# Kernel optimization log

Measured on AMD Instinct MI355X. Metric: run time of the kernel, lower is better.

Reference implementation:

```python
import jax, jax.numpy as jnp
import numpy as np

B, J, C = 256, 21, 256   # batch, joints, in_dim
H, D = 8, 256            # heads, out_dim (=hidden)
L, K = 2, 8              # layers, knn_k


def _knn_idx(coords, k):
    # coords: (B,J,3). Squared distances give same ordering as cdist p=2.
    d2 = jnp.sum((coords[:, :, None, :] - coords[:, None, :, :]) ** 2, axis=-1)  # (B,J,J)
    order = jnp.argsort(d2, axis=-1)
    return order[..., 1:k + 1]  # drop self -> (B,J,K)


def _mhgat(x, nbr_idx, wq, wk, wv, wp):
    b, j, _ = x.shape
    q = (x @ wq).reshape(b, j, H, D)
    k = (x @ wk).reshape(b, j, H, D)
    v = (x @ wv).reshape(b, j, H, D)
    bi = jnp.arange(b)[:, None, None]
    k_nbr = k[bi, nbr_idx]  # (B,J,K,H,D) gather of neighbor keys
    v_nbr = v[bi, nbr_idx]  # (B,J,K,H,D)
    attn = jnp.einsum('bjhd,bjkhd->bjkh', q, k_nbr) / np.float32(np.sqrt(D))
    attn = jax.nn.leaky_relu(attn, negative_slope=0.2)
    attn = jax.nn.softmax(attn, axis=2)  # over K neighbors
    out = jnp.einsum('bjkh,bjkhd->bjhd', attn, v_nbr).reshape(b, j, H * D)
    return out @ wp  # (B,J,hidden)


def setup_inputs() -> dict:
    key = jax.random.key(0)
    ks = jax.random.split(key, 9)
    s_in = 1.0 / np.sqrt(C)
    s_hd = 1.0 / np.sqrt(H * D)
    s_h = 1.0 / np.sqrt(D)
    joint_feats = jax.random.normal(ks[0], (B, J, C), jnp.float32)
    # layer-stacked weights (in_dim == hidden == 256 so both layers stack)
    wq = jax.random.normal(ks[1], (L, C, H * D), jnp.float32) * s_in
    wk = jax.random.normal(ks[2], (L, C, H * D), jnp.float32) * s_in
    wv = jax.random.normal(ks[3], (L, C, H * D), jnp.float32) * s_in
    wp = jax.random.normal(ks[4], (L, H * D, D), jnp.float32) * s_hd
    ws = jax.random.normal(ks[5], (L, C, D), jnp.float32) * s_in
    wskip0 = jax.random.normal(ks[6], (C, D), jnp.float32) * s_in
    fc_w = jax.random.normal(ks[7], (D, 3), jnp.float32) * s_h
    fc_b = jax.random.normal(ks[8], (3,), jnp.float32) * s_h
    return {"joint_feats": joint_feats, "wq": wq, "wk": wk, "wv": wv,
            "wp": wp, "ws": ws, "wskip0": wskip0, "fc_w": fc_w, "fc_b": fc_b}


def reference(joint_feats, wq, wk, wv, wp, ws, wskip0, fc_w, fc_b):
    h0 = joint_feats
    h = h0
    stats = []
    for l in range(L):
        nbr_idx = _knn_idx(jax.lax.stop_gradient(h[..., :3]), K)  # dynamic kNN graph
        out = _mhgat(h, nbr_idx, wq[l], wk[l], wv[l], wp[l])
        h = jax.nn.relu(out + h @ ws[l] + h0 @ wskip0)
        stats.append(jnp.abs(h).mean())
    coords = h @ fc_w + fc_b
    alphas = jnp.mean(jnp.stack(stats))
    return coords, alphas
```

## Files before the change

kernel.cpp:

```cpp
#include <hip/hip_runtime.h>
#include <hip/hip_bf16.h>
#include <math.h>
#include <type_traits>

namespace {
constexpr int Bb = 256, Jj = 21, Cc = 256, Hh = 8, Dd = 256;
constexpr int Mrows = Bb * Jj;
constexpr int HD    = Hh * Dd;
constexpr int QKVN  = 3 * HD;
constexpr int KNN   = 8;
constexpr int KFUSE = HD + Cc + Cc;

constexpr size_t OFF_QKV   = 0;
constexpr size_t OFF_T     = OFF_QKV   + (size_t)Mrows*QKVN*2;
constexpr size_t OFF_ATT   = OFF_T     + (size_t)Mrows*HD*4;
constexpr size_t OFF_GT    = OFF_ATT   + (size_t)Mrows*HD*2;
constexpr size_t OFF_G1T   = OFF_GT    + (size_t)HD*768*2;
constexpr size_t OFF_JFB   = OFF_G1T   + (size_t)HD*Cc*2;
constexpr size_t OFF_JFH   = OFF_JFB   + (size_t)Mrows*Cc*2;
constexpr size_t OFF_JFL   = OFF_JFH   + (size_t)Mrows*Cc*2;
constexpr size_t OFF_JFD   = OFF_JFL   + (size_t)Mrows*Cc*2;
constexpr size_t OFF_H1B   = OFF_JFD   + (size_t)Mrows*Cc*2;
constexpr size_t OFF_H2F   = OFF_H1B   + (size_t)Mrows*Cc*2;
constexpr size_t OFF_WQKVT = OFF_H2F   + (size_t)Mrows*Cc*4;
constexpr size_t OFF_FBT   = OFF_WQKVT + (size_t)2*QKVN*Cc*2;
constexpr size_t OFF_WVP   = OFF_FBT   + (size_t)2*Cc*KFUSE*2;
constexpr size_t OFF_VPROJ = OFF_WVP   + (size_t)Cc*24*4;
constexpr size_t OFF_WSUM  = OFF_VPROJ + (size_t)Mrows*24*4;
constexpr size_t OFF_CRD   = OFF_WSUM  + (size_t)Cc*4*4;
constexpr size_t OFF_NBR0  = OFF_CRD   + (size_t)Mrows*4*4;
constexpr size_t OFF_NBR1  = OFF_NBR0  + (size_t)Mrows*KNN*4;
constexpr size_t OFF_STAT  = OFF_NBR1  + (size_t)Mrows*KNN*4;
}

typedef short short8 __attribute__((ext_vector_type(8)));
typedef _Float16 half8 __attribute__((ext_vector_type(8)));
typedef _Float16 half4v __attribute__((ext_vector_type(4)));
typedef unsigned short u16x8 __attribute__((ext_vector_type(8)));
typedef float f32x4 __attribute__((ext_vector_type(4)));

__device__ __forceinline__ unsigned short f2bf(float x) {
    unsigned int u = __float_as_uint(x);
    u = u + 0x7fffu + ((u >> 16) & 1u);
    return (unsigned short)(u >> 16);
}
__device__ __forceinline__ float bf2f(unsigned short b) {
    return __uint_as_float(((unsigned int)b) << 16);
}

__device__ __forceinline__ void knn_body(int b, const float* __restrict__ src,
                                         int ld, int* __restrict__ nbr,
                                         float (*cs)[3]) {
    int t = threadIdx.x;
    if (t < Jj) {
        const float* p = src + (size_t)(b * Jj + t) * ld;
        cs[t][0] = p[0]; cs[t][1] = p[1]; cs[t][2] = p[2];
    }
    __syncthreads();
    if (t < Jj) {
        float x = cs[t][0], y = cs[t][1], z = cs[t][2];
        float d2[Jj];
        #pragma unroll
        for (int jj = 0; jj < Jj; ++jj) {
            float dx = x - cs[jj][0], dy = y - cs[jj][1], dz = z - cs[jj][2];
            d2[jj] = dx*dx + dy*dy + dz*dz;
        }
        unsigned int used = 0u;
        int out_base = (b * Jj + t) * KNN;
        #pragma unroll
        for (int r = 0; r <= KNN; ++r) {
            int best = -1; float bd = INFINITY;
            #pragma unroll
            for (int jj = 0; jj < Jj; ++jj)
                if (!((used >> jj) & 1u) && d2[jj] < bd) { bd = d2[jj]; best = jj; }
            used |= (1u << best);
            if (r > 0) nbr[out_base + r - 1] = best;
        }
    }
}

__device__ __forceinline__ void g_gemm_body(const float* __restrict__ wq,
                                            const float* __restrict__ wk,
                                            int h, int m0, int n0, char* sm,
                                            float acc[2][4]) {
    float (*As)[36] = (float(*)[36])sm;
    float (*Ws)[68] = (float(*)[68])(sm + 4608);
    int tidx = threadIdx.x;
    int ty = tidx >> 4, tx = tidx & 15;
    for (int kb = 0; kb < 256; kb += 32) {
        {
            int row = tidx >> 3, col = (tidx & 7) * 4;
            float4 v = *(const float4*)&wq[(size_t)(m0 + row)*HD + h*256 + kb + col];
            As[col+0][row] = v.x; As[col+1][row] = v.y;
            As[col+2][row] = v.z; As[col+3][row] = v.w;
            int row2 = tidx >> 2, col2 = (tidx & 3) * 8;
            float4 u0 = *(const float4*)&wk[(size_t)(n0 + row2)*HD + h*256 + kb + col2];
            float4 u1 = *(const float4*)&wk[(size_t)(n0 + row2)*HD + h*256 + kb + col2 + 4];
            Ws[col2+0][row2] = u0.x; Ws[col2+1][row2] = u0.y;
            Ws[col2+2][row2] = u0.z; Ws[col2+3][row2] = u0.w;
            Ws[col2+4][row2] = u1.x; Ws[col2+5][row2] = u1.y;
            Ws[col2+6][row2] = u1.z; Ws[col2+7][row2] = u1.w;
        }
        __syncthreads();
        #pragma unroll
        for (int kk = 0; kk < 32; ++kk) {
            float a0 = As[kk][ty*2], a1 = As[kk][ty*2 + 1];
            float4 bv = *(const float4*)&Ws[kk][tx*4];
            float b4[4] = {bv.x, bv.y, bv.z, bv.w};
            #pragma unroll
            for (int j = 0; j < 4; ++j) {
                acc[0][j] += a0 * b4[j];
                acc[1][j] += a1 * b4[j];
            }
        }
        __syncthreads();
    }
}

__global__ __launch_bounds__(256)
void mega_prep_kernel(const float* __restrict__ jf,
                      const float* __restrict__ wq, const float* __restrict__ wk,
                      const float* __restrict__ wv, const float* __restrict__ wp,
                      const float* __restrict__ wsw, const float* __restrict__ wsk,
                      unsigned short* __restrict__ wqkvT,
                      unsigned short* __restrict__ fbt, float* __restrict__ stats,
                      float* __restrict__ wsum,
                      unsigned short* __restrict__ jfb, _Float16* __restrict__ jfh,
                      _Float16* __restrict__ jfl, _Float16* __restrict__ jfd,
                      _Float16* __restrict__ GT, unsigned short* __restrict__ G1T,
                      float* __restrict__ Wvp2, int* __restrict__ nbr0) {
    __shared__ __align__(16) char sm[17408];
    int bid = blockIdx.x;
    int tidx = threadIdx.x;
    constexpr size_t CH = (size_t)Cc * HD;

    if (bid < 256) {
        int h = bid >> 5, rem = bid & 31;
        int m0 = (rem >> 2) * 32, n0 = (rem & 3) * 64;
        int ty = tidx >> 4, tx = tidx & 15;
        float acc[2][4] = {};
        g_gemm_body(wq, wk, h, m0, n0, sm, acc);
        #pragma unroll
        for (int j = 0; j < 4; ++j) {
            int n = h*256 + n0 + tx*4 + j;
            float g0 = acc[0][j], g1 = acc[1][j];
            _Float16 h0_ = (_Float16)g0, h1_ = (_Float16)g1;
            _Float16* base = &GT[(size_t)n*768 + m0 + ty*2];
            base[0]   = h0_;                          base[1]   = h1_;
            base[256] = (_Float16)(g0 * 0.0625f);     base[257] = (_Float16)(g1 * 0.0625f);
            base[512] = (_Float16)((g0 - (float)h0_) * 128.0f);
            base[513] = (_Float16)((g1 - (float)h1_) * 128.0f);
        }
    } else if (bid < 512) {
        int q = bid - 256;
        int h = q >> 5, rem = q & 31;
        int m0 = (rem >> 2) * 32, n0 = (rem & 3) * 64;
        int ty = tidx >> 4, tx = tidx & 15;
        float acc[2][4] = {};
        g_gemm_body(wq + CH, wk + CH, h, m0, n0, sm, acc);
        #pragma unroll
        for (int j = 0; j < 4; ++j) {
            int n = h*256 + n0 + tx*4 + j;
            unsigned short* base = &G1T[(size_t)n*256 + m0 + ty*2];
            base[0] = f2bf(acc[0][j]);
            base[1] = f2bf(acc[1][j]);
        }
    } else if (bid < 520) {
        int h = bid - 512;
        float (*wpc)[3] = (float(*)[3])sm;
        int t = tidx;
        const float* p = &wp[(size_t)(h*256 + t) * Cc];
        wpc[t][0] = p[0]; wpc[t][1] = p[1]; wpc[t][2] = p[2];
        __syncthreads();
        const float* vr = &wv[(size_t)t*HD + h*256];
        float a0=0, a1=0, a2=0;
        for (int d = 0; d < 256; ++d) {
            float v = vr[d];
            a0 += v*wpc[d][0]; a1 += v*wpc[d][1]; a2 += v*wpc[d][2];
        }
        float* o = &Wvp2[(size_t)t*24 + h*3];
        o[0]=a0; o[1]=a1; o[2]=a2;
    } else if (bid < 776) {
        knn_body(bid - 520, jf, Cc, nbr0, (float(*)[3])sm);
    } else if (bid == 776) {
        int e = tidx;
        float4 o;
        o.x = wsw[(size_t)e*Dd + 0] + wsk[(size_t)e*Dd + 0];
        o.y = wsw[(size_t)e*Dd + 1] + wsk[(size_t)e*Dd + 1];
        o.z = wsw[(size_t)e*Dd + 2] + wsk[(size_t)e*Dd + 2];
        o.w = 0.0f;
        *(float4*)&wsum[e*4] = o;
        if (e < 2) stats[e] = 0.0f;
    } else if (bid < 2121) {
        int i = (bid - 777) * 256 + tidx;
        float4 v = ((const float4*)jf)[i];
        float x[4] = {v.x, v.y, v.z, v.w};
        ushort4 ob; half4v oh, ol, od;
        #pragma unroll
        for (int u = 0; u < 4; ++u) {
            ((unsigned short*)&ob)[u] = f2bf(x[u]);
            _Float16 h = (_Float16)x[u];
            oh[u] = h;
            ol[u] = (_Float16)((x[u] - (float)h) * 16.0f);
            od[u] = (_Float16)(x[u] * 0.0078125f);
        }
        ((ushort4*)jfb)[i] = ob;
        ((half4v*)jfh)[i] = oh;
        ((half4v*)jfl)[i] = ol;
        ((half4v*)jfd)[i] = od;
    } else {
        int tt = bid - 2121;
        const float* src; unsigned short* dst;
        int ldin, ldout, tilesX, tile;
        if (tt < 2048) {
            int opIdx = tt >> 9; tile = tt & 511; tilesX = 64;
            int op = (opIdx < 3) ? opIdx : 5;
            ldin = HD; ldout = Cc;
            const float* s3[3] = {wq, wk, wv};
            src = s3[op % 3] + (size_t)(op / 3) * CH;
            dst = wqkvT + (size_t)(op % 3) * HD * Cc + (size_t)(op / 3) * QKVN * Cc;
        } else if (tt < 3072) {
            int op = (tt - 2048) >> 9; tile = (tt - 2048) & 511; tilesX = 8;
            ldin = Cc; ldout = KFUSE;
            src = wp + (size_t)op * HD * Cc;
            dst = fbt + (size_t)op * Cc * KFUSE;
        } else {
            int q = tt - 3072; int op = q >> 6; tile = q & 63; tilesX = 8;
            ldin = Cc; ldout = KFUSE;
            const float* s4[4] = {wsw, wsw + (size_t)Cc * Cc, wsk, wsk};
            src = s4[op];
            dst = fbt + (size_t)(op & 1) * Cc * KFUSE + HD + (size_t)(op >> 1) * Cc;
        }
        int bx = tile % tilesX, by = tile / tilesX;
        int n0 = bx * 32, k0 = by * 32;
        float (*t)[33] = (float(*)[33])sm;
        int r = tidx >> 3, c4 = (tidx & 7) * 4;
        float4 v = *(const float4*)&src[(size_t)(k0 + r) * ldin + n0 + c4];
        t[r][c4+0] = v.x; t[r][c4+1] = v.y; t[r][c4+2] = v.z; t[r][c4+3] = v.w;
        __syncthreads();
        ushort4 o;
        o.x = f2bf(t[c4+0][r]); o.y = f2bf(t[c4+1][r]);
        o.z = f2bf(t[c4+2][r]); o.w = f2bf(t[c4+3][r]);
        *(ushort4*)&dst[(size_t)(n0 + r) * ldout + k0 + c4] = o;
    }
}

template<int BM, int BN, int BK, int NSEG, bool RELU_STATS, bool OUT_BF16, bool F16>
__device__ __forceinline__
void gemm_core(unsigned short* As, unsigned short* Bs, float* red,
               int bm, int bn,
               const unsigned short* __restrict__ A0, int lda0, int klen0,
               const unsigned short* __restrict__ A1, int lda1, int klen1,
               const unsigned short* __restrict__ A2, int lda2, int klen2,
               const unsigned short* __restrict__ Bt, int ldb,
               void* __restrict__ Cv, int ldc, float* __restrict__ stat) {
    constexpr int WM = BM/2, WN = BN/2;
    constexpr int MW = WM/16, NW = WN/16, KW = BK/32;
    constexpr int CHUNKA = BM*BK/8;
    constexpr int CHUNKB = BN*BK/8;
    constexpr int KB8 = BK/8;
    constexpr int SWZ = KB8 - 1;
    using frag = std::conditional_t<F16, half8, short8>;

    int tid = threadIdx.x;
    int wid = tid >> 6, lane = tid & 63;
    int wr = wid >> 1, wc = wid & 1;

    f32x4 acc[MW][NW];
    #pragma unroll
    for (int m = 0; m < MW; ++m)
        #pragma unroll
        for (int n = 0; n < NW; ++n)
            acc[m][n] = (f32x4){0.f, 0.f, 0.f, 0.f};

    const unsigned short* Aseg[3] = {A0, A1, A2};
    const int ldas[3] = {lda0, lda1, lda2};
    const int klens[3] = {klen0, klen1, klen2};

    int kglob = 0;
    for (int seg = 0; seg < NSEG; ++seg) {
        const unsigned short* A = Aseg[seg];
        const int lda = ldas[seg];
        const int klen = klens[seg];
        for (int k0 = 0; k0 < klen; k0 += BK) {
            #pragma unroll
            for (int it = 0; it < CHUNKA/256; ++it) {
                int c = tid + it*256;
                int row = c / KB8;
                int kp = (c % KB8) ^ (row & SWZ);
                __builtin_amdgcn_global_load_lds(
                    (const __attribute__((address_space(1))) unsigned int*)
                        (A + (size_t)(bm + row)*lda + k0 + kp*8),
                    (__attribute__((address_space(3))) unsigned int*)(As + c*8),
                    16, 0, 0);
            }
            #pragma unroll
            for (int it = 0; it < CHUNKB/256; ++it) {
                int c = tid + it*256;
                int row = c / KB8;
                int kp = (c % KB8) ^ (row & SWZ);
                __builtin_amdgcn_global_load_lds(
                    (const __attribute__((address_space(1))) unsigned int*)
                        (Bt + (size_t)(bn + row)*ldb + kglob + k0 + kp*8),
                    (__attribute__((address_space(3))) unsigned int*)(Bs + c*8),
                    16, 0, 0);
            }
            __syncthreads();
            #pragma unroll
            for (int kp = 0; kp < KW; ++kp) {
                frag af[MW], bf[NW];
                int cbase = kp*4 + (lane >> 4);
                #pragma unroll
                for (int m = 0; m < MW; ++m) {
                    int r = wr*WM + m*16 + (lane & 15);
                    af[m] = *(const frag*)&As[r*BK + ((cbase ^ (r & SWZ))*8)];
                }
                #pragma unroll
                for (int n = 0; n < NW; ++n) {
                    int r = wc*WN + n*16 + (lane & 15);
                    bf[n] = *(const frag*)&Bs[r*BK + ((cbase ^ (r & SWZ))*8)];
                }
                #pragma unroll
                for (int m = 0; m < MW; ++m)
                    #pragma unroll
                    for (int n = 0; n < NW; ++n) {
                        if constexpr (F16)
                            acc[m][n] = __builtin_amdgcn_mfma_f32_16x16x32_f16(
                                af[m], bf[n], acc[m][n], 0, 0, 0);
                        else
                            acc[m][n] = __builtin_amdgcn_mfma_f32_16x16x32_bf16(
                                af[m], bf[n], acc[m][n], 0, 0, 0);
                    }
            }
            __syncthreads();
        }
        kglob += klen;
    }

    int cr = (lane >> 4)*4, cc = lane & 15;
    float bsum = 0.0f;
    #pragma unroll
    for (int m = 0; m < MW; ++m)
        #pragma unroll
        for (int n = 0; n < NW; ++n)
            #pragma unroll
            for (int j = 0; j < 4; ++j) {
                float v = acc[m][n][j];
                if (RELU_STATS) { v = fmaxf(v, 0.0f); bsum += v; }
                size_t row = bm + wr*WM + m*16 + cr + j;
                size_t col = bn + wc*WN + n*16 + cc;
                if (OUT_BF16) ((unsigned short*)Cv)[row*ldc + col] = f2bf(v);
                else          ((float*)Cv)[row*ldc + col] = v;
            }
    if (RELU_STATS) {
        #pragma unroll
        for (int sft = 1; sft < 64; sft <<= 1) bsum += __shfl_xor(bsum, sft);
        if (lane == 0) red[wid] = bsum;
        __syncthreads();
        if (tid == 0) atomicAdd(stat, red[0] + red[1] + red[2] + red[3]);
    }
}

__global__ __launch_bounds__(256)
void combo_kernel(const unsigned short* __restrict__ jfb,
                  const unsigned short* __restrict__ wqkvT,
                  unsigned short* __restrict__ QKVb,
                  const _Float16* __restrict__ jfh, const _Float16* __restrict__ jfl,
                  const _Float16* __restrict__ jfd, const _Float16* __restrict__ GT,
                  float* __restrict__ Tm,
                  const float* __restrict__ jf, const float* __restrict__ Wvp2,
                  float* __restrict__ vproj) {
    __shared__ __align__(16) char smem[32784];
    unsigned short* As = (unsigned short*)smem;
    unsigned short* Bs = (unsigned short*)(smem + 16384);
    float* red = (float*)(smem + 32768);
    int x = blockIdx.x, y = blockIdx.y;
    if (y < 16) {
        int lb = x + 42*y;
        int nb = (lb & 7) * 84 + (lb >> 3);
        int sx = nb % 42, sy = nb / 42;
        gemm_core<128,128,64,1,false,true,false>(As, Bs, red, sx*128,
            2*HD + sy*128,
            jfb, Cc, Cc, jfb, Cc, 0, jfb, Cc, 0, wqkvT, Cc, QKVb, QKVN, nullptr);
    } else if (y < 32) {
        int lb = x + 42*(y - 16);
        int nb = (lb & 7) * 84 + (lb >> 3);
        int sx = nb / 16, sy = nb % 16;
        gemm_core<128,128,64,3,false,false,true>(As, Bs, red, sx*128, sy*128,
            (const unsigned short*)jfh, Cc, Cc, (const unsigned short*)jfl, Cc, Cc,
            (const unsigned short*)jfd, Cc, Cc, (const unsigned short*)GT, 768,
            Tm, HD, nullptr);
    } else {
        int q = (y - 32) * 42 + x;
        float (*hr)[256] = (float(*)[256])smem;
        float* wl = (float*)(smem + 8192);
        int t = threadIdx.x;
        int j0 = q * 8;
        #pragma unroll
        for (int i = 0; i < 6; ++i)
            *(float4*)&wl[t*4 + i*1024] = *(const float4*)&Wvp2[t*4 + i*1024];
        {
            int r = t >> 5, c = (t & 31) * 8;
            const float* src = &jf[(size_t)(j0 + r)*Cc + c];
            *(float4*)&hr[r][c]   = *(const float4*)src;
            *(float4*)&hr[r][c+4] = *(const float4*)(src + 4);
        }
        __syncthreads();
        int r = t >> 5, o = t & 31;
        if (o < 24) {
            float a = 0.0f;
            for (int e = 0; e < 256; ++e) a += hr[r][e] * wl[e*24 + o];
            vproj[(size_t)(j0 + r)*24 + o] = a;
        }
    }
}

__global__ __launch_bounds__(256)
void combo1_kernel(const unsigned short* __restrict__ h1b,
                   const unsigned short* __restrict__ wqkvT1,
                   const unsigned short* __restrict__ G1T,
                   unsigned short* __restrict__ QKVb) {
    __shared__ __align__(16) unsigned short As[128*64];
    __shared__ __align__(16) unsigned short Bs[128*64];
    __shared__ float red[4];
    int x = blockIdx.x, y = blockIdx.y;
    if (y < 16) {
        int lb = x + 42*y;
        int nb = (lb & 7) * 84 + (lb >> 3);
        int sx = nb % 42, sy = nb / 42;
        gemm_core<128,128,64,1,false,true,false>(As, Bs, red, sx*128,
            2*HD + sy*128,
            h1b, Cc, Cc, h1b, Cc, 0, h1b, Cc, 0, wqkvT1, Cc, QKVb, QKVN, nullptr);
    } else {
        int lb = x + 42*(y - 16);
        int nb = (lb & 7) * 84 + (lb >> 3);
        int sx = nb % 42, sy = nb / 42;
        gemm_core<128,128,64,1,false,true,false>(As, Bs, red, sx*128, sy*128,
            h1b, Cc, Cc, h1b, Cc, 0, h1b, Cc, 0, G1T, Cc, QKVb, QKVN, nullptr);
    }
}

template<bool OUT_BF16, bool DO_KNN>
__global__ __launch_bounds__(256)
void fused_kernel(const unsigned short* __restrict__ att,
                  const unsigned short* __restrict__ hseg,
                  const unsigned short* __restrict__ h0seg,
                  const unsigned short* __restrict__ fbtL,
                  void* __restrict__ Cv, float* __restrict__ stat,
                  const float* __restrict__ crd, int* __restrict__ nbr1) {
    __shared__ __align__(16) char smem[16400];
    if (DO_KNN && blockIdx.y >= 4) {
        int b = (blockIdx.y - 4) * 84 + blockIdx.x;
        if (b < Bb) knn_body(b, crd, 4, nbr1, (float(*)[3])smem);
        return;
    }
    unsigned short* As = (unsigned short*)smem;
    unsigned short* Bs = (unsigned short*)(smem + 8192);
    float* red = (float*)(smem + 16384);
    gemm_core<64,64,64,3,true,OUT_BF16,false>(
        As, Bs, red, blockIdx.x*64, blockIdx.y*64,
        att, HD, HD, hseg, Cc, Cc, h0seg, Cc, Cc,
        fbtL, KFUSE, Cv, Cc, stat);
}

__global__ __launch_bounds__(64)
void precise_kernel(const float* __restrict__ T, const float* __restrict__ h0,
                    const int* __restrict__ nbr, const float* __restrict__ vproj,
                    const float* __restrict__ wsum,
                    const unsigned short* __restrict__ QKV,
                    float* __restrict__ crd, unsigned short* __restrict__ att) {
    int lb = blockIdx.x;
    int i = (lb & 7) * (Mrows/8) + (lb >> 3);
    int b = i / Jj;
    int l = threadIdx.x;
    __shared__ float Ts[8][260];
    __shared__ float nb[8][260];
    __shared__ float hi[256];
    __shared__ float wsL[64];
    __shared__ int nbs[KNN];
    #pragma unroll
    for (int u = 0; u < 8; ++u) {
        int idx = u*64 + l;
        float4 v = *(const float4*)&T[(size_t)i*HD + idx*4];
        int hh = idx >> 6, dd = (idx & 63) * 4;
        *(float4*)&Ts[hh][dd] = v;
    }
    *(float4*)&hi[l*4] = *(const float4*)&h0[(size_t)i*Cc + l*4];
    if (l < KNN) nbs[l] = nbr[i*KNN + l];
    int kq = l >> 3, s = l & 7;
    int njs = nbr[i*KNN + kq];
    const float* nrow = &h0[(size_t)(b*Jj + njs)*Cc];
    #pragma unroll
    for (int u = 0; u < 8; ++u)
        *(float4*)&nb[kq][(s*8+u)*4] = *(const float4*)&nrow[(s*8+u)*4];
    __syncthreads();

    int k = l >> 3, h = l & 7;
    float sacc = 0;
    #pragma unroll 8
    for (int d = 0; d < 256; d += 4) {
        float4 tv = *(const float4*)&Ts[h][d];
        float4 nv = *(const float4*)&nb[k][d];
        sacc += tv.x*nv.x + tv.y*nv.y + tv.z*nv.z + tv.w*nv.w;
    }
    float sc = sacc * 0.0625f;
    sc = (sc >= 0.0f) ? sc : 0.2f * sc;
    float m = sc;
    m = fmaxf(m, __shfl_xor(m, 8));
    m = fmaxf(m, __shfl_xor(m, 16));
    m = fmaxf(m, __shfl_xor(m, 32));
    float e = expf(sc - m);
    float den = e;
    den += __shfl_xor(den, 8); den += __shfl_xor(den, 16); den += __shfl_xor(den, 32);
    float w = e / den;
    wsL[l] = w;

    int njk = nbs[k];
    const float* vp = &vproj[(size_t)(b*Jj + njk)*24 + h*3];
    float t0 = w * vp[0], t1 = w * vp[1], t2 = w * vp[2];
    #pragma unroll
    for (int u = 0; u < 4; ++u) {
        int e4 = l*4 + u;
        float hv = hi[e4];
        float4 wv = *(const float4*)&wsum[e4*4];
        t0 += hv * wv.x; t1 += hv * wv.y; t2 += hv * wv.z;
    }
    #pragma unroll
    for (int sft = 1; sft < 64; sft <<= 1) {
        t0 += __shfl_xor(t0, sft); t1 += __shfl_xor(t1, sft); t2 += __shfl_xor(t2, sft);
    }
    if (l == 0) {
        crd[i*4+0] = fmaxf(t0, 0.0f);
        crd[i*4+1] = fmaxf(t1, 0.0f);
        crd[i*4+2] = fmaxf(t2, 0.0f);
        crd[i*4+3] = 0.0f;
    }
    __syncthreads();

    int h2 = l >> 3, sub = l & 7;
    float o[32] = {};
    #pragma unroll
    for (int kk = 0; kk < KNN; ++kk) {
        float wk_ = wsL[kk*8 + h2];
        const unsigned short* vrow =
            &QKV[(size_t)(b*Jj + nbs[kk])*QKVN + 2*HD + h2*256 + sub*32];
        #pragma unroll
        for (int j = 0; j < 4; ++j) {
            u16x8 v = *(const u16x8*)(vrow + j*8);
            #pragma unroll
            for (int u = 0; u < 8; ++u) o[j*8+u] += wk_ * bf2f(v[u]);
        }
    }
    unsigned short* arow = &att[(size_t)i*HD + h2*256 + sub*32];
    #pragma unroll
    for (int j = 0; j < 4; ++j) {
        u16x8 ou;
        #pragma unroll
        for (int u = 0; u < 8; ++u) ou[u] = f2bf(o[j*8+u]);
        *(u16x8*)(arow + j*8) = ou;
    }
}

__global__ __launch_bounds__(64)
void attn1_kernel(const unsigned short* __restrict__ QKV,
                  const unsigned short* __restrict__ h1b,
                  const int* __restrict__ nbr, unsigned short* __restrict__ att) {
    int lb = blockIdx.x;
    int gid = (lb & 7) * (Mrows*4/8) + (lb >> 3);
    int hp = gid & 3, row = gid >> 2, b = row / Jj;
    int lane = threadIdx.x;
    int h = hp*2 + (lane >> 5);
    int d0 = (lane & 31) * 8;

    u16x8 tu = *(const u16x8*)&QKV[(size_t)row*QKVN + h*Dd + d0];
    float tf[8];
    #pragma unroll
    for (int i = 0; i < 8; ++i) tf[i] = bf2f(tu[i]);
    const int* np_ = nbr + row * KNN;

    float sc[KNN]; int nb[KNN];
    #pragma unroll
    for (int k = 0; k < KNN; ++k) {
        int n = np_[k]; nb[k] = n;
        u16x8 hu = *(const u16x8*)&h1b[(size_t)(b*Jj + n)*Cc + d0];
        float p = 0;
        #pragma unroll
        for (int i = 0; i < 8; ++i) p += tf[i] * bf2f(hu[i]);
        #pragma unroll
        for (int s = 1; s < 32; s <<= 1) p += __shfl_xor(p, s);
        sc[k] = p;
    }
    float mx = -INFINITY;
    #pragma unroll
    for (int k = 0; k < KNN; ++k) {
        float s = sc[k] * 0.0625f;
        s = (s >= 0.0f) ? s : 0.2f * s;
        sc[k] = s; mx = fmaxf(mx, s);
    }
    float den = 0.0f;
    #pragma unroll
    for (int k = 0; k < KNN; ++k) { sc[k] = expf(sc[k] - mx); den += sc[k]; }
    float inv = 1.0f / den;
    float o[8] = {};
    #pragma unroll
    for (int k = 0; k < KNN; ++k) {
        u16x8 vu = *(const u16x8*)&QKV[(size_t)(b*Jj + nb[k])*QKVN + 2*HD + h*Dd + d0];
        float w = sc[k] * inv;
        #pragma unroll
        for (int i = 0; i < 8; ++i) o[i] += w * bf2f(vu[i]);
    }
    u16x8 ou;
    #pragma unroll
    for (int i = 0; i < 8; ++i) ou[i] = f2bf(o[i]);
    *(u16x8*)&att[(size_t)row*HD + h*Dd + d0] = ou;
}

__global__ __launch_bounds__(64)
void final_kernel(const float* __restrict__ h, const float* __restrict__ fcw,
                  const float* __restrict__ fcb, const float* __restrict__ stats,
                  float* __restrict__ out) {
    int row = blockIdx.x, lane = threadIdx.x;
    const float4 hv = *(const float4*)(h + (size_t)row*Cc + lane*4);
    float a0=0, a1=0, a2=0;
    const float hx[4] = {hv.x, hv.y, hv.z, hv.w};
    #pragma unroll
    for (int i = 0; i < 4; ++i) {
        int c = lane*4 + i;
        a0 += hx[i]*fcw[c*3+0]; a1 += hx[i]*fcw[c*3+1]; a2 += hx[i]*fcw[c*3+2];
    }
    #pragma unroll
    for (int s = 32; s > 0; s >>= 1) {
        a0 += __shfl_xor(a0, s); a1 += __shfl_xor(a1, s); a2 += __shfl_xor(a2, s);
    }
    if (lane == 0) {
        out[row*3+0] = a0 + fcb[0];
        out[row*3+1] = a1 + fcb[1];
        out[row*3+2] = a2 + fcb[2];
        if (row == 0)
            out[(size_t)Mrows*3] =
                (stats[0] + stats[1]) * (0.5f / ((float)Mrows * (float)Cc));
    }
}

extern "C" void kernel_launch(void* const* d_in, const int* in_sizes, int n_in,
                              void* d_out, int out_size, void* d_ws, size_t ws_size,
                              hipStream_t stream) {
    (void)in_sizes; (void)n_in; (void)out_size; (void)ws_size;
    const float* jf     = (const float*)d_in[0];
    const float* wq     = (const float*)d_in[1];
    const float* wk     = (const float*)d_in[2];
    const float* wv     = (const float*)d_in[3];
    const float* wp     = (const float*)d_in[4];
    const float* wsw    = (const float*)d_in[5];
    const float* wskip0 = (const float*)d_in[6];
    const float* fcw    = (const float*)d_in[7];
    const float* fcb    = (const float*)d_in[8];
    float* out = (float*)d_out;

    char* wsb = (char*)d_ws;
    unsigned short* QKVb  = (unsigned short*)(wsb + OFF_QKV);
    float*          Tm    = (float*)(wsb + OFF_T);
    unsigned short* attb  = (unsigned short*)(wsb + OFF_ATT);
    _Float16*       GT    = (_Float16*)(wsb + OFF_GT);
    unsigned short* G1T   = (unsigned short*)(wsb + OFF_G1T);
    unsigned short* jfb   = (unsigned short*)(wsb + OFF_JFB);
    _Float16*       jfh   = (_Float16*)(wsb + OFF_JFH);
    _Float16*       jfl   = (_Float16*)(wsb + OFF_JFL);
    _Float16*       jfd   = (_Float16*)(wsb + OFF_JFD);
    unsigned short* h1b   = (unsigned short*)(wsb + OFF_H1B);
    float*          h2f   = (float*)(wsb + OFF_H2F);
    unsigned short* wqkvT = (unsigned short*)(wsb + OFF_WQKVT);
    unsigned short* fbt   = (unsigned short*)(wsb + OFF_FBT);
    float*          Wvp   = (float*)(wsb + OFF_WVP);
    float*          vproj = (float*)(wsb + OFF_VPROJ);
    float*          wsum  = (float*)(wsb + OFF_WSUM);
    float*          crd   = (float*)(wsb + OFF_CRD);
    int*            nbr0  = (int*)(wsb + OFF_NBR0);
    int*            nbr1  = (int*)(wsb + OFF_NBR1);
    float*          stats = (float*)(wsb + OFF_STAT);

    mega_prep_kernel<<<5449, 256, 0, stream>>>(jf, wq, wk, wv, wp, wsw, wskip0,
                                               wqkvT, fbt, stats, wsum,
                                               jfb, jfh, jfl, jfd, GT, G1T,
                                               Wvp, nbr0);
    combo_kernel<<<dim3(42, 48), 256, 0, stream>>>(jfb, wqkvT, QKVb,
                                                   jfh, jfl, jfd, GT, Tm,
                                                   jf, Wvp, vproj);
    precise_kernel<<<Mrows, 64, 0, stream>>>(Tm, jf, nbr0, vproj, wsum,
                                             QKVb, crd, attb);
    fused_kernel<true, true><<<dim3(84, 8), 256, 0, stream>>>(
        attb, jfb, jfb, fbt, h1b, &stats[0], crd, nbr1);
    combo1_kernel<<<dim3(42, 32), 256, 0, stream>>>(
        h1b, wqkvT + (size_t)QKVN*Cc, G1T, QKVb);
    attn1_kernel<<<Mrows*4, 64, 0, stream>>>(QKVb, h1b, nbr1, attb);
    fused_kernel<false, false><<<dim3(84, 4), 256, 0, stream>>>(
        attb, h1b, jfb, fbt + (size_t)Cc*KFUSE, h2f, &stats[1], nullptr, nullptr);
    final_kernel<<<Mrows, 64, 0, stream>>>(h2f, fcw, fcb, stats, out);
}
```

Baseline: 191.5 us.

## Pre-sum layer-0 skip weights to drop one GEMM segment, swizzle fused tiles

Since layer 0 input equals h0, the skip and self weights are summed during weight prep, so the layer-0 fused GEMM runs over two K segments instead of three. The fused GEMM blocks get a swizzled tile mapping for better cache locality. precise_kernel keeps h0 values in registers instead of staging them through shared memory. Adding weights in fp32 before the bf16 conversion slightly changes rounding. The new block mapping assumes a particular grid shape.

```diff
diff --git a/kernel.cpp b/kernel.cpp
--- a/kernel.cpp
+++ b/kernel.cpp
@@ -9,7 +9,8 @@
 constexpr int HD    = Hh * Dd;
 constexpr int QKVN  = 3 * HD;
 constexpr int KNN   = 8;
-constexpr int KFUSE = HD + Cc + Cc;
+constexpr int KF0   = HD + Cc;
+constexpr int KF1   = HD + 2*Cc;
 
 constexpr size_t OFF_QKV   = 0;
 constexpr size_t OFF_T     = OFF_QKV   + (size_t)Mrows*QKVN*2;
@@ -23,8 +24,9 @@
 constexpr size_t OFF_H1B   = OFF_JFD   + (size_t)Mrows*Cc*2;
 constexpr size_t OFF_H2F   = OFF_H1B   + (size_t)Mrows*Cc*2;
 constexpr size_t OFF_WQKVT = OFF_H2F   + (size_t)Mrows*Cc*4;
-constexpr size_t OFF_FBT   = OFF_WQKVT + (size_t)2*QKVN*Cc*2;
-constexpr size_t OFF_WVP   = OFF_FBT   + (size_t)2*Cc*KFUSE*2;
+constexpr size_t OFF_FBT0  = OFF_WQKVT + (size_t)2*QKVN*Cc*2;
+constexpr size_t OFF_FBT1  = OFF_FBT0  + (size_t)Cc*KF0*2;
+constexpr size_t OFF_WVP   = OFF_FBT1  + (size_t)Cc*KF1*2;
 constexpr size_t OFF_VPROJ = OFF_WVP   + (size_t)Cc*24*4;
 constexpr size_t OFF_WSUM  = OFF_VPROJ + (size_t)Mrows*24*4;
 constexpr size_t OFF_CRD   = OFF_WSUM  + (size_t)Cc*4*4;
@@ -123,8 +125,9 @@
                       const float* __restrict__ wv, const float* __restrict__ wp,
                       const float* __restrict__ wsw, const float* __restrict__ wsk,
                       unsigned short* __restrict__ wqkvT,
-                      unsigned short* __restrict__ fbt, float* __restrict__ stats,
-                      float* __restrict__ wsum,
+                      unsigned short* __restrict__ fbt0,
+                      unsigned short* __restrict__ fbt1,
+                      float* __restrict__ stats, float* __restrict__ wsum,
                       unsigned short* __restrict__ jfb, _Float16* __restrict__ jfh,
                       _Float16* __restrict__ jfl, _Float16* __restrict__ jfd,
                       _Float16* __restrict__ GT, unsigned short* __restrict__ G1T,
@@ -210,7 +213,8 @@
         ((half4v*)jfd)[i] = od;
     } else {
         int tt = bid - 2121;
-        const float* src; unsigned short* dst;
+        const float* src = nullptr; const float* src2 = nullptr;
+        unsigned short* dst;
         int ldin, ldout, tilesX, tile;
         if (tt < 2048) {
             int opIdx = tt >> 9; tile = tt & 511; tilesX = 64;
@@ -219,23 +223,31 @@
             const float* s3[3] = {wq, wk, wv};
             src = s3[op % 3] + (size_t)(op / 3) * CH;
             dst = wqkvT + (size_t)(op % 3) * HD * Cc + (size_t)(op / 3) * QKVN * Cc;
+        } else if (tt < 2560) {
+            tile = tt - 2048; tilesX = 8; ldin = Cc; ldout = KF0;
+            src = wp; dst = fbt0;
         } else if (tt < 3072) {
-            int op = (tt - 2048) >> 9; tile = (tt - 2048) & 511; tilesX = 8;
-            ldin = Cc; ldout = KFUSE;
-            src = wp + (size_t)op * HD * Cc;
-            dst = fbt + (size_t)op * Cc * KFUSE;
+            tile = tt - 2560; tilesX = 8; ldin = Cc; ldout = KF1;
+            src = wp + CH; dst = fbt1;
+        } else if (tt < 3136) {
+            tile = tt - 3072; tilesX = 8; ldin = Cc; ldout = KF0;
+            src = wsw; src2 = wsk; dst = fbt0 + HD;
+        } else if (tt < 3200) {
+            tile = tt - 3136; tilesX = 8; ldin = Cc; ldout = KF1;
+            src = wsw + (size_t)Cc * Cc; dst = fbt1 + HD;
         } else {
-            int q = tt - 3072; int op = q >> 6; tile = q & 63; tilesX = 8;
-            ldin = Cc; ldout = KFUSE;
-            const float* s4[4] = {wsw, wsw + (size_t)Cc * Cc, wsk, wsk};
-            src = s4[op];
-            dst = fbt + (size_t)(op & 1) * Cc * KFUSE + HD + (size_t)(op >> 1) * Cc;
+            tile = tt - 3200; tilesX = 8; ldin = Cc; ldout = KF1;
+            src = wsk; dst = fbt1 + HD + Cc;
         }
         int bx = tile % tilesX, by = tile / tilesX;
         int n0 = bx * 32, k0 = by * 32;
         float (*t)[33] = (float(*)[33])sm;
         int r = tidx >> 3, c4 = (tidx & 7) * 4;
         float4 v = *(const float4*)&src[(size_t)(k0 + r) * ldin + n0 + c4];
+        if (src2) {
+            float4 w = *(const float4*)&src2[(size_t)(k0 + r) * ldin + n0 + c4];
+            v.x += w.x; v.y += w.y; v.z += w.z; v.w += w.w;
+        }
         t[r][c4+0] = v.x; t[r][c4+1] = v.y; t[r][c4+2] = v.z; t[r][c4+3] = v.w;
         __syncthreads();
         ushort4 o;
@@ -440,12 +452,12 @@
     }
 }
 
-template<bool OUT_BF16, bool DO_KNN>
+template<int NSEG, bool OUT_BF16, bool DO_KNN>
 __global__ __launch_bounds__(256)
 void fused_kernel(const unsigned short* __restrict__ att,
-                  const unsigned short* __restrict__ hseg,
-                  const unsigned short* __restrict__ h0seg,
-                  const unsigned short* __restrict__ fbtL,
+                  const unsigned short* __restrict__ hseg, int hk,
+                  const unsigned short* __restrict__ h0seg, int h0k,
+                  const unsigned short* __restrict__ fbtL, int ldb,
                   void* __restrict__ Cv, float* __restrict__ stat,
                   const float* __restrict__ crd, int* __restrict__ nbr1) {
     __shared__ __align__(16) char smem[16400];
@@ -457,10 +469,13 @@
     unsigned short* As = (unsigned short*)smem;
     unsigned short* Bs = (unsigned short*)(smem + 8192);
     float* red = (float*)(smem + 16384);
-    gemm_core<64,64,64,3,true,OUT_BF16,false>(
-        As, Bs, red, blockIdx.x*64, blockIdx.y*64,
-        att, HD, HD, hseg, Cc, Cc, h0seg, Cc, Cc,
-        fbtL, KFUSE, Cv, Cc, stat);
+    int idx = blockIdx.x * 4 + blockIdx.y;
+    int nb = (idx & 7) * 42 + (idx >> 3);
+    int sx = nb >> 2, sy = nb & 3;
+    gemm_core<64,64,64,NSEG,true,OUT_BF16,false>(
+        As, Bs, red, sx*64, sy*64,
+        att, HD, HD, hseg, Cc, hk, h0seg, Cc, h0k,
+        fbtL, ldb, Cv, Cc, stat);
 }
 
 __global__ __launch_bounds__(64)
@@ -475,7 +490,6 @@
     int l = threadIdx.x;
     __shared__ float Ts[8][260];
     __shared__ float nb[8][260];
-    __shared__ float hi[256];
     __shared__ float wsL[64];
     __shared__ int nbs[KNN];
     #pragma unroll
@@ -485,7 +499,7 @@
         int hh = idx >> 6, dd = (idx & 63) * 4;
         *(float4*)&Ts[hh][dd] = v;
     }
-    *(float4*)&hi[l*4] = *(const float4*)&h0[(size_t)i*Cc + l*4];
+    float4 hv4 = *(const float4*)&h0[(size_t)i*Cc + l*4];
     if (l < KNN) nbs[l] = nbr[i*KNN + l];
     int kq = l >> 3, s = l & 7;
     int njs = nbr[i*KNN + kq];
@@ -518,12 +532,11 @@
     int njk = nbs[k];
     const float* vp = &vproj[(size_t)(b*Jj + njk)*24 + h*3];
     float t0 = w * vp[0], t1 = w * vp[1], t2 = w * vp[2];
+    const float hx[4] = {hv4.x, hv4.y, hv4.z, hv4.w};
     #pragma unroll
     for (int u = 0; u < 4; ++u) {
-        int e4 = l*4 + u;
-        float hv = hi[e4];
-        float4 wv = *(const float4*)&wsum[e4*4];
-        t0 += hv * wv.x; t1 += hv * wv.y; t2 += hv * wv.z;
+        float4 wv = *(const float4*)&wsum[(l*4 + u)*4];
+        t0 += hx[u] * wv.x; t1 += hx[u] * wv.y; t2 += hx[u] * wv.z;
     }
     #pragma unroll
     for (int sft = 1; sft < 64; sft <<= 1) {
@@ -670,7 +683,8 @@
     unsigned short* h1b   = (unsigned short*)(wsb + OFF_H1B);
     float*          h2f   = (float*)(wsb + OFF_H2F);
     unsigned short* wqkvT = (unsigned short*)(wsb + OFF_WQKVT);
-    unsigned short* fbt   = (unsigned short*)(wsb + OFF_FBT);
+    unsigned short* fbt0  = (unsigned short*)(wsb + OFF_FBT0);
+    unsigned short* fbt1  = (unsigned short*)(wsb + OFF_FBT1);
     float*          Wvp   = (float*)(wsb + OFF_WVP);
     float*          vproj = (float*)(wsb + OFF_VPROJ);
     float*          wsum  = (float*)(wsb + OFF_WSUM);
@@ -679,8 +693,8 @@
     int*            nbr1  = (int*)(wsb + OFF_NBR1);
     float*          stats = (float*)(wsb + OFF_STAT);
 
-    mega_prep_kernel<<<5449, 256, 0, stream>>>(jf, wq, wk, wv, wp, wsw, wskip0,
-                                               wqkvT, fbt, stats, wsum,
+    mega_prep_kernel<<<5385, 256, 0, stream>>>(jf, wq, wk, wv, wp, wsw, wskip0,
+                                               wqkvT, fbt0, fbt1, stats, wsum,
                                                jfb, jfh, jfl, jfd, GT, G1T,
                                                Wvp, nbr0);
     combo_kernel<<<dim3(42, 48), 256, 0, stream>>>(jfb, wqkvT, QKVb,
@@ -688,12 +702,12 @@
                                                    jf, Wvp, vproj);
     precise_kernel<<<Mrows, 64, 0, stream>>>(Tm, jf, nbr0, vproj, wsum,
                                              QKVb, crd, attb);
-    fused_kernel<true, true><<<dim3(84, 8), 256, 0, stream>>>(
-        attb, jfb, jfb, fbt, h1b, &stats[0], crd, nbr1);
+    fused_kernel<2, true, true><<<dim3(84, 8), 256, 0, stream>>>(
+        attb, jfb, Cc, jfb, 0, fbt0, KF0, h1b, &stats[0], crd, nbr1);
     combo1_kernel<<<dim3(42, 32), 256, 0, stream>>>(
         h1b, wqkvT + (size_t)QKVN*Cc, G1T, QKVb);
     attn1_kernel<<<Mrows*4, 64, 0, stream>>>(QKVb, h1b, nbr1, attb);
-    fused_kernel<false, false><<<dim3(84, 4), 256, 0, stream>>>(
-        attb, h1b, jfb, fbt + (size_t)Cc*KFUSE, h2f, &stats[1], nullptr, nullptr);
+    fused_kernel<3, false, false><<<dim3(84, 4), 256, 0, stream>>>(
+        attb, h1b, Cc, jfb, Cc, fbt1, KF1, h2f, &stats[1], nullptr, nullptr);
     final_kernel<<<Mrows, 64, 0, stream>>>(h2f, fcw, fcb, stats, out);
 }
```

Measured after the change: 189.2 us. About the same (-1.2%).
